# Optimization experiments

Measured on AMD Instinct MI355X. Metric: run time of the kernel, lower is better.

Reference implementation:

```python
import jax, jax.numpy as jnp
from jax import lax
import numpy as np

HID = 512
BATCH = 4096
T = 20
OUT = 1


def setup_inputs() -> dict:
    key = jax.random.key(0)
    ks = jax.random.split(key, 10)
    s = 1.0 / np.sqrt(HID)
    y = jax.random.normal(ks[0], (BATCH, HID), dtype=jnp.float32)
    ts = jnp.arange(T, dtype=jnp.float32) * 0.1  # time grid
    Wi = jax.random.uniform(ks[1], (HID, HID), jnp.float32, -s, s)
    Wf = jax.random.uniform(ks[2], (HID, HID), jnp.float32, -s, s)
    Wg = jax.random.uniform(ks[3], (HID, HID), jnp.float32, -s, s)
    Wo = jax.random.uniform(ks[4], (HID, HID), jnp.float32, -s, s)
    Wout = jax.random.uniform(ks[5], (HID, HID), jnp.float32, -s, s)
    bout = jax.random.uniform(ks[6], (HID,), jnp.float32, -s, s)
    Wfc = jax.random.uniform(ks[7], (OUT, HID), jnp.float32, -s, s)
    bfc = jax.random.uniform(ks[8], (OUT,), jnp.float32, -s, s)
    return {"y": y, "ts": ts, "Wi": Wi, "Wf": Wf, "Wg": Wg, "Wo": Wo,
            "Wout": Wout, "bout": bout, "Wfc": Wfc, "bfc": bfc}


def reference(y, ts, Wi, Wf, Wg, Wo, Wout, bout, Wfc, bfc):
    def odefunc(z):  # z: [B, H]
        i = jax.nn.sigmoid(z @ Wi.T)
        f = jax.nn.sigmoid(z @ Wf.T)  # computed (as in source) but unused in dh
        g = jnp.tanh(z @ Wg.T)
        o = jax.nn.sigmoid(z @ Wo.T)
        dh = o * jnp.tanh(i * g)
        return jax.nn.softmax(dh @ Wout.T + bout, axis=1)

    def euler_step(z, dt):
        z_next = z + dt * odefunc(z)
        return z_next, z_next

    dts = ts[1:] - ts[:-1]
    _, zs = lax.scan(euler_step, y, dts)          # [T-1, B, H]
    zt = jnp.concatenate([y[None], zs], axis=0)   # [T, B, H]
    zt = jax.nn.softmax(zt, axis=2).transpose(1, 0, 2)  # [B, T, H]
    out = zt @ Wfc.T + bfc                        # [B, T, 1]
    return out.squeeze(2)                         # [B, T]
```

## Files before the change

kernel.cpp:

```cpp
#include <hip/hip_runtime.h>
#include <cstdint>
#include <cstddef>

#define HID 512
#define BATCH 4096
#define T_STEPS 20

typedef unsigned short ushort_t;
typedef __attribute__((ext_vector_type(8))) __bf16 bf16x8;
typedef __attribute__((ext_vector_type(4))) float f32x4;

typedef __attribute__((address_space(1))) void gvoid;
typedef __attribute__((address_space(3))) void lvoid;

__device__ __forceinline__ unsigned short f2bf(float f) {
  unsigned int u = __float_as_uint(f);
  u += 0x7FFFu + ((u >> 16) & 1u);
  return (unsigned short)(u >> 16);
}

__device__ __forceinline__ void load_lds16(const void* g, void* l) {
  __builtin_amdgcn_global_load_lds((gvoid*)g, (lvoid*)l, 16, 0, 0);
}

#define WAITV6 do { asm volatile("s_waitcnt vmcnt(6)" ::: "memory"); __builtin_amdgcn_sched_barrier(0); } while (0)
#define WAITV4 do { asm volatile("s_waitcnt vmcnt(4)" ::: "memory"); __builtin_amdgcn_sched_barrier(0); } while (0)
#define WAITV0 do { asm volatile("s_waitcnt vmcnt(0)" ::: "memory"); __builtin_amdgcn_sched_barrier(0); } while (0)

__device__ __forceinline__ float frcp(float x) {
  float r; asm("v_rcp_f32 %0, %1" : "=v"(r) : "v"(x)); return r;
}
__device__ __forceinline__ float fsigm(float x) { return frcp(1.f + __expf(-x)); }
__device__ __forceinline__ float ftanh(float x) { return 1.f - 2.f * frcp(__expf(2.f * x) + 1.f); }

__global__ __launch_bounds__(512) void ode_persistent(
    const float* __restrict__ y,
    const ushort_t* __restrict__ Wcat,
    const ushort_t* __restrict__ WoutB,
    const float* __restrict__ bout,
    const float* __restrict__ Wfc, const float* __restrict__ bfc,
    const float* __restrict__ ts, float* __restrict__ out) {
  __shared__ ushort_t wst[2][8][3072];
  __shared__ ushort_t zbs[64 * 16 * 8];
  __shared__ ushort_t dhs[64 * 16 * 8];
  __shared__ float rmax1[8][16];
  __shared__ float rsum1[8][16];
  __shared__ float rmax2[8][16];
  __shared__ float rsd[8][16][2];
  __shared__ float dts[T_STEPS];

  const int tid = threadIdx.x;
  const int wave = tid >> 6;
  const int lane = tid & 63;
  const int quad = lane >> 4;
  const int l16 = lane & 15;
  const int m0 = blockIdx.x * 16;
  const int wn2 = wave * 64;

  if (tid < T_STEPS - 1) dts[tid] = ts[tid + 1] - ts[tid];

  float boutr[4], wfcr[4];
#pragma unroll
  for (int j = 0; j < 4; ++j) {
    boutr[j] = bout[wn2 + j * 16 + l16];
    wfcr[j] = Wfc[wn2 + j * 16 + l16];
  }
  const float bfc0 = bfc[0];

  ushort_t* const w0 = &wst[0][wave][0];
  ushort_t* const w1 = &wst[1][wave][0];

  int loff1[6];
#pragma unroll
  for (int i = 0; i < 6; ++i) {
    int c = (i & 1) * 8 + (lane >> 3);
    int kc = (lane & 7) ^ (c & 7);
    loff1[i] = (i >> 1) * 262144 + (wave * 16 + c) * 512 + kc * 8;
  }
  int loff2[4];
#pragma unroll
  for (int i = 0; i < 4; ++i) {
    int c = i * 16 + (lane >> 2);
    int kc = (lane & 3) ^ ((lane >> 3) & 3);
    loff2[i] = (wave * 64 + c) * 512 + kc * 8;
  }
  const int x7 = l16 & 7;
  const int x3b = (l16 >> 1) & 3;

  f32x4 zreg[4];
#pragma unroll
  for (int j = 0; j < 4; ++j) {
    int col = wn2 + j * 16 + l16;
    int kp = col >> 3, ce = col & 7;
#pragma unroll
    for (int r = 0; r < 4; ++r) {
      float v = y[(size_t)(m0 + quad * 4 + r) * HID + col];
      zreg[j][r] = v;
      zbs[(kp * 16 + quad * 4 + r) * 8 + ce] = f2bf(v);
    }
  }

  auto proj_out = [&](int tcol) {
    float m2[4];
#pragma unroll
    for (int r = 0; r < 4; ++r) {
      float m = zreg[0][r];
#pragma unroll
      for (int j = 1; j < 4; ++j) m = fmaxf(m, zreg[j][r]);
#pragma unroll
      for (int off = 1; off < 16; off <<= 1) m = fmaxf(m, __shfl_xor(m, off));
      m2[r] = m;
    }
    if (l16 == 0) {
#pragma unroll
      for (int r = 0; r < 4; ++r) rmax2[wave][quad * 4 + r] = m2[r];
    }
    __syncthreads();
#pragma unroll
    for (int r = 0; r < 4; ++r) {
      int row = quad * 4 + r;
      float m = rmax2[0][row];
#pragma unroll
      for (int w = 1; w < 8; ++w) m = fmaxf(m, rmax2[w][row]);
      m2[r] = m;
    }
    float s2[4] = {0.f, 0.f, 0.f, 0.f};
    float dd[4] = {0.f, 0.f, 0.f, 0.f};
#pragma unroll
    for (int j = 0; j < 4; ++j)
#pragma unroll
      for (int r = 0; r < 4; ++r) {
        float e = __expf(zreg[j][r] - m2[r]);
        s2[r] += e;
        dd[r] += e * wfcr[j];
      }
#pragma unroll
    for (int r = 0; r < 4; ++r) {
#pragma unroll
      for (int off = 1; off < 16; off <<= 1) {
        s2[r] += __shfl_xor(s2[r], off);
        dd[r] += __shfl_xor(dd[r], off);
      }
    }
    if (l16 == 0) {
#pragma unroll
      for (int r = 0; r < 4; ++r) {
        rsd[wave][quad * 4 + r][0] = s2[r];
        rsd[wave][quad * 4 + r][1] = dd[r];
      }
    }
    __syncthreads();
    if (wave == 0 && l16 == 0) {
#pragma unroll
      for (int r = 0; r < 4; ++r) {
        int row = quad * 4 + r;
        float ss = 0.f, dv = 0.f;
#pragma unroll
        for (int w = 0; w < 8; ++w) { ss += rsd[w][row][0]; dv += rsd[w][row][1]; }
        out[(size_t)(m0 + row) * T_STEPS + tcol] = dv / ss + bfc0;
      }
    }
    __syncthreads();
  };

  auto stage1n = [&](ushort_t* dst, int nt) {
    const ushort_t* pt = Wcat + ((nt >> 3) << 16) + ((nt & 7) << 6);
#pragma unroll
    for (int i = 0; i < 6; ++i)
      load_lds16(pt + loff1[i], dst + i * 512);
  };
  auto stage2n = [&](ushort_t* dst, int nt) {
    const ushort_t* pt = WoutB + nt * 32;
#pragma unroll
    for (int i = 0; i < 4; ++i)
      load_lds16(pt + loff2[i], dst + i * 512);
  };

  proj_out(0);

  for (int t = 0; t < T_STEPS - 1; ++t) {
    bf16x8 afr[16];
#pragma unroll
    for (int kk = 0; kk < 8; ++kk) {
      afr[2 * kk]     = *(const bf16x8*)&zbs[((kk * 8 + quad) * 16 + l16) * 8];
      afr[2 * kk + 1] = *(const bf16x8*)&zbs[((kk * 8 + 4 + quad) * 16 + l16) * 8];
    }

    stage1n(w0, 0);
#pragma unroll 1
    for (int ht = 0; ht < 4; ++ht) {
      f32x4 a0 = {}, a1 = {}, a2 = {};
#pragma unroll
      for (int kk = 0; kk < 8; ++kk) {
        ushort_t* wc = (kk & 1) ? w1 : w0;
        ushort_t* wn = (kk & 1) ? w0 : w1;
        if (kk < 7) {
          stage1n(wn, ht * 8 + kk + 1); WAITV6;
        } else if (ht < 3) {
          stage1n(wn, ht * 8 + 8); WAITV6;
        } else {
          WAITV0;
        }
        bf16x8 b00 = *(const bf16x8*)&wc[(0 * 128 + l16 * 8 + (quad ^ x7)) * 8];
        bf16x8 b01 = *(const bf16x8*)&wc[(0 * 128 + l16 * 8 + ((quad + 4) ^ x7)) * 8];
        bf16x8 b10 = *(const bf16x8*)&wc[(1 * 128 + l16 * 8 + (quad ^ x7)) * 8];
        bf16x8 b11 = *(const bf16x8*)&wc[(1 * 128 + l16 * 8 + ((quad + 4) ^ x7)) * 8];
        bf16x8 b20 = *(const bf16x8*)&wc[(2 * 128 + l16 * 8 + (quad ^ x7)) * 8];
        bf16x8 b21 = *(const bf16x8*)&wc[(2 * 128 + l16 * 8 + ((quad + 4) ^ x7)) * 8];
        a0 = __builtin_amdgcn_mfma_f32_16x16x32_bf16(afr[2 * kk], b00, a0, 0, 0, 0);
        a0 = __builtin_amdgcn_mfma_f32_16x16x32_bf16(afr[2 * kk + 1], b01, a0, 0, 0, 0);
        a1 = __builtin_amdgcn_mfma_f32_16x16x32_bf16(afr[2 * kk], b10, a1, 0, 0, 0);
        a1 = __builtin_amdgcn_mfma_f32_16x16x32_bf16(afr[2 * kk + 1], b11, a1, 0, 0, 0);
        a2 = __builtin_amdgcn_mfma_f32_16x16x32_bf16(afr[2 * kk], b20, a2, 0, 0, 0);
        a2 = __builtin_amdgcn_mfma_f32_16x16x32_bf16(afr[2 * kk + 1], b21, a2, 0, 0, 0);
      }
      {
        int col = ht * 128 + wave * 16 + l16;
        int kp = col >> 3, ce = col & 7;
#pragma unroll
        for (int r = 0; r < 4; ++r) {
          float gi = fsigm(a0[r]);
          float gg = ftanh(a1[r]);
          float go = fsigm(a2[r]);
          dhs[(kp * 16 + quad * 4 + r) * 8 + ce] = f2bf(go * ftanh(gi * gg));
        }
      }
    }
    __syncthreads();

    f32x4 acc2[4] = {};
    stage2n(w0, 0);
#pragma unroll
    for (int tt = 0; tt < 16; ++tt) {
      ushort_t* wc = (tt & 1) ? w1 : w0;
      ushort_t* wn = (tt & 1) ? w0 : w1;
      if (tt + 1 < 16) { stage2n(wn, tt + 1); WAITV4; } else { WAITV0; }
      bf16x8 afd = *(const bf16x8*)&dhs[((tt * 4 + quad) * 16 + l16) * 8];
#pragma unroll
      for (int j = 0; j < 4; ++j) {
        bf16x8 bf = *(const bf16x8*)&wc[(((j * 16 + l16) * 4) + (quad ^ x3b)) * 8];
        acc2[j] = __builtin_amdgcn_mfma_f32_16x16x32_bf16(afd, bf, acc2[j], 0, 0, 0);
      }
    }

    const float dtv = dts[t];
#pragma unroll
    for (int j = 0; j < 4; ++j)
#pragma unroll
      for (int r = 0; r < 4; ++r) acc2[j][r] += boutr[j];

    float m1[4];
#pragma unroll
    for (int r = 0; r < 4; ++r) {
      float m = acc2[0][r];
#pragma unroll
      for (int j = 1; j < 4; ++j) m = fmaxf(m, acc2[j][r]);
#pragma unroll
      for (int off = 1; off < 16; off <<= 1) m = fmaxf(m, __shfl_xor(m, off));
      m1[r] = m;
    }
    if (l16 == 0) {
#pragma unroll
      for (int r = 0; r < 4; ++r) rmax1[wave][quad * 4 + r] = m1[r];
    }
    __syncthreads();
#pragma unroll
    for (int r = 0; r < 4; ++r) {
      int row = quad * 4 + r;
      float m = rmax1[0][row];
#pragma unroll
      for (int w = 1; w < 8; ++w) m = fmaxf(m, rmax1[w][row]);
      m1[r] = m;
    }

    float s1[4] = {0.f, 0.f, 0.f, 0.f};
#pragma unroll
    for (int j = 0; j < 4; ++j)
#pragma unroll
      for (int r = 0; r < 4; ++r) {
        float e = __expf(acc2[j][r] - m1[r]);
        acc2[j][r] = e;
        s1[r] += e;
      }
#pragma unroll
    for (int r = 0; r < 4; ++r) {
#pragma unroll
      for (int off = 1; off < 16; off <<= 1) s1[r] += __shfl_xor(s1[r], off);
    }
    if (l16 == 0) {
#pragma unroll
      for (int r = 0; r < 4; ++r) rsum1[wave][quad * 4 + r] = s1[r];
    }
    __syncthreads();
    float inv1[4];
#pragma unroll
    for (int r = 0; r < 4; ++r) {
      int row = quad * 4 + r;
      float s = rsum1[0][row];
#pragma unroll
      for (int w = 1; w < 8; ++w) s += rsum1[w][row];
      inv1[r] = 1.f / s;
    }

#pragma unroll
    for (int j = 0; j < 4; ++j) {
      int col = wn2 + j * 16 + l16;
      int kp = col >> 3, ce = col & 7;
#pragma unroll
      for (int r = 0; r < 4; ++r) {
        float zn = zreg[j][r] + dtv * acc2[j][r] * inv1[r];
        zreg[j][r] = zn;
        zbs[(kp * 16 + quad * 4 + r) * 8 + ce] = f2bf(zn);
      }
    }

    proj_out(t + 1);
  }
}

__global__ __launch_bounds__(256) void convw_kernel(
    const float* __restrict__ Wi, const float* __restrict__ Wg,
    const float* __restrict__ Wo, const float* __restrict__ Wout,
    ushort_t* __restrict__ Wcat, ushort_t* __restrict__ WoutB) {
  const int nW = HID * HID;
  int e = (blockIdx.x * 256 + threadIdx.x) * 4;
  const float* src;
  ushort_t* dst;
  if (e < nW)            { src = Wi + e;          dst = Wcat + e; }
  else if (e < 2 * nW)   { src = Wg + (e - nW);   dst = Wcat + e; }
  else if (e < 3 * nW)   { src = Wo + (e - 2*nW); dst = Wcat + e; }
  else                   { src = Wout + (e - 3*nW); dst = WoutB + (e - 3*nW); }
  float4 v = *(const float4*)src;
  union { unsigned short us[4]; uint2 u; } p;
  p.us[0] = f2bf(v.x); p.us[1] = f2bf(v.y); p.us[2] = f2bf(v.z); p.us[3] = f2bf(v.w);
  *(uint2*)dst = p.u;
}

extern "C" void kernel_launch(void* const* d_in, const int* in_sizes, int n_in,
                              void* d_out, int out_size, void* d_ws, size_t ws_size,
                              hipStream_t stream) {
  const float* y    = (const float*)d_in[0];
  const float* ts   = (const float*)d_in[1];
  const float* Wi   = (const float*)d_in[2];
  const float* Wg   = (const float*)d_in[4];
  const float* Wo   = (const float*)d_in[5];
  const float* Wout = (const float*)d_in[6];
  const float* bout = (const float*)d_in[7];
  const float* Wfc  = (const float*)d_in[8];
  const float* bfc  = (const float*)d_in[9];
  float* out = (float*)d_out;

  char* ws = (char*)d_ws;
  ushort_t* Wcat  = (ushort_t*)(ws);
  ushort_t* WoutB = (ushort_t*)(ws + 1572864);

  convw_kernel<<<1024, 256, 0, stream>>>(Wi, Wg, Wo, Wout, Wcat, WoutB);
  ode_persistent<<<256, 512, 0, stream>>>(y, Wcat, WoutB, bout, Wfc, bfc, ts, out);
}
```

Measured before the change: 678.9 us.

## Load weight fragments directly into registers with triple-buffered global loads instead of LDS staging

```diff
diff --git a/kernel.cpp b/kernel.cpp
--- a/kernel.cpp
+++ b/kernel.cpp
@@ -9,9 +9,6 @@
 typedef unsigned short ushort_t;
 typedef __attribute__((ext_vector_type(8))) __bf16 bf16x8;
 typedef __attribute__((ext_vector_type(4))) float f32x4;
-
-typedef __attribute__((address_space(1))) void gvoid;
-typedef __attribute__((address_space(3))) void lvoid;
 
 __device__ __forceinline__ unsigned short f2bf(float f) {
   unsigned int u = __float_as_uint(f);
@@ -19,19 +16,24 @@
   return (unsigned short)(u >> 16);
 }
 
-__device__ __forceinline__ void load_lds16(const void* g, void* l) {
-  __builtin_amdgcn_global_load_lds((gvoid*)g, (lvoid*)l, 16, 0, 0);
-}
-
-#define WAITV6 do { asm volatile("s_waitcnt vmcnt(6)" ::: "memory"); __builtin_amdgcn_sched_barrier(0); } while (0)
-#define WAITV4 do { asm volatile("s_waitcnt vmcnt(4)" ::: "memory"); __builtin_amdgcn_sched_barrier(0); } while (0)
-#define WAITV0 do { asm volatile("s_waitcnt vmcnt(0)" ::: "memory"); __builtin_amdgcn_sched_barrier(0); } while (0)
-
 __device__ __forceinline__ float frcp(float x) {
   float r; asm("v_rcp_f32 %0, %1" : "=v"(r) : "v"(x)); return r;
 }
 __device__ __forceinline__ float fsigm(float x) { return frcp(1.f + __expf(-x)); }
 __device__ __forceinline__ float ftanh(float x) { return 1.f - 2.f * frcp(__expf(2.f * x) + 1.f); }
+
+__device__ __forceinline__ bf16x8 gload(const ushort_t* base, int voff) {
+  bf16x8 r;
+  asm volatile("global_load_dwordx4 %0, %1, %2"
+               : "=v"(r) : "v"(voff), "s"(base) : "memory");
+  return r;
+}
+
+#define WAIT12 do { asm volatile("s_waitcnt vmcnt(12)" ::: "memory"); __builtin_amdgcn_sched_barrier(0); } while (0)
+#define WAIT8  do { asm volatile("s_waitcnt vmcnt(8)"  ::: "memory"); __builtin_amdgcn_sched_barrier(0); } while (0)
+#define WAIT6  do { asm volatile("s_waitcnt vmcnt(6)"  ::: "memory"); __builtin_amdgcn_sched_barrier(0); } while (0)
+#define WAIT4  do { asm volatile("s_waitcnt vmcnt(4)"  ::: "memory"); __builtin_amdgcn_sched_barrier(0); } while (0)
+#define WAIT0  do { asm volatile("s_waitcnt vmcnt(0)"  ::: "memory"); __builtin_amdgcn_sched_barrier(0); } while (0)
 
 __global__ __launch_bounds__(512) void ode_persistent(
     const float* __restrict__ y,
@@ -40,7 +42,6 @@
     const float* __restrict__ bout,
     const float* __restrict__ Wfc, const float* __restrict__ bfc,
     const float* __restrict__ ts, float* __restrict__ out) {
-  __shared__ ushort_t wst[2][8][3072];
   __shared__ ushort_t zbs[64 * 16 * 8];
   __shared__ ushort_t dhs[64 * 16 * 8];
   __shared__ float rmax1[8][16];
@@ -67,25 +68,16 @@
   }
   const float bfc0 = bfc[0];
 
-  ushort_t* const w0 = &wst[0][wave][0];
-  ushort_t* const w1 = &wst[1][wave][0];
-
-  int loff1[6];
+  int voff1[6];
 #pragma unroll
   for (int i = 0; i < 6; ++i) {
-    int c = (i & 1) * 8 + (lane >> 3);
-    int kc = (lane & 7) ^ (c & 7);
-    loff1[i] = (i >> 1) * 262144 + (wave * 16 + c) * 512 + kc * 8;
+    int gate = i >> 1, half = i & 1;
+    voff1[i] = 2 * (gate * 262144 + (wave * 16 + l16) * 512 + half * 32 + quad * 8);
   }
-  int loff2[4];
-#pragma unroll
-  for (int i = 0; i < 4; ++i) {
-    int c = i * 16 + (lane >> 2);
-    int kc = (lane & 3) ^ ((lane >> 3) & 3);
-    loff2[i] = (wave * 64 + c) * 512 + kc * 8;
-  }
-  const int x7 = l16 & 7;
-  const int x3b = (l16 >> 1) & 3;
+  int voff2[4];
+#pragma unroll
+  for (int j = 0; j < 4; ++j)
+    voff2[j] = 2 * ((wave * 64 + j * 16 + l16) * 512 + quad * 8);
 
   f32x4 zreg[4];
 #pragma unroll
@@ -163,19 +155,6 @@
     __syncthreads();
   };
 
-  auto stage1n = [&](ushort_t* dst, int nt) {
-    const ushort_t* pt = Wcat + ((nt >> 3) << 16) + ((nt & 7) << 6);
-#pragma unroll
-    for (int i = 0; i < 6; ++i)
-      load_lds16(pt + loff1[i], dst + i * 512);
-  };
-  auto stage2n = [&](ushort_t* dst, int nt) {
-    const ushort_t* pt = WoutB + nt * 32;
-#pragma unroll
-    for (int i = 0; i < 4; ++i)
-      load_lds16(pt + loff2[i], dst + i * 512);
-  };
-
   proj_out(0);
 
   for (int t = 0; t < T_STEPS - 1; ++t) {
@@ -186,36 +165,37 @@
       afr[2 * kk + 1] = *(const bf16x8*)&zbs[((kk * 8 + 4 + quad) * 16 + l16) * 8];
     }
 
-    stage1n(w0, 0);
-#pragma unroll 1
-    for (int ht = 0; ht < 4; ++ht) {
-      f32x4 a0 = {}, a1 = {}, a2 = {};
-#pragma unroll
-      for (int kk = 0; kk < 8; ++kk) {
-        ushort_t* wc = (kk & 1) ? w1 : w0;
-        ushort_t* wn = (kk & 1) ? w0 : w1;
-        if (kk < 7) {
-          stage1n(wn, ht * 8 + kk + 1); WAITV6;
-        } else if (ht < 3) {
-          stage1n(wn, ht * 8 + 8); WAITV6;
-        } else {
-          WAITV0;
-        }
-        bf16x8 b00 = *(const bf16x8*)&wc[(0 * 128 + l16 * 8 + (quad ^ x7)) * 8];
-        bf16x8 b01 = *(const bf16x8*)&wc[(0 * 128 + l16 * 8 + ((quad + 4) ^ x7)) * 8];
-        bf16x8 b10 = *(const bf16x8*)&wc[(1 * 128 + l16 * 8 + (quad ^ x7)) * 8];
-        bf16x8 b11 = *(const bf16x8*)&wc[(1 * 128 + l16 * 8 + ((quad + 4) ^ x7)) * 8];
-        bf16x8 b20 = *(const bf16x8*)&wc[(2 * 128 + l16 * 8 + (quad ^ x7)) * 8];
-        bf16x8 b21 = *(const bf16x8*)&wc[(2 * 128 + l16 * 8 + ((quad + 4) ^ x7)) * 8];
-        a0 = __builtin_amdgcn_mfma_f32_16x16x32_bf16(afr[2 * kk], b00, a0, 0, 0, 0);
-        a0 = __builtin_amdgcn_mfma_f32_16x16x32_bf16(afr[2 * kk + 1], b01, a0, 0, 0, 0);
-        a1 = __builtin_amdgcn_mfma_f32_16x16x32_bf16(afr[2 * kk], b10, a1, 0, 0, 0);
-        a1 = __builtin_amdgcn_mfma_f32_16x16x32_bf16(afr[2 * kk + 1], b11, a1, 0, 0, 0);
-        a2 = __builtin_amdgcn_mfma_f32_16x16x32_bf16(afr[2 * kk], b20, a2, 0, 0, 0);
-        a2 = __builtin_amdgcn_mfma_f32_16x16x32_bf16(afr[2 * kk + 1], b21, a2, 0, 0, 0);
-      }
+    bf16x8 bb[3][6];
+#pragma unroll
+    for (int p = 0; p < 3; ++p) {
+      const int d = (p >> 3) * 131072 + (p & 7) * 128;
+#pragma unroll
+      for (int i = 0; i < 6; ++i) bb[p][i] = gload(Wcat, voff1[i] + d);
+    }
+    f32x4 a0 = {}, a1 = {}, a2 = {};
+#pragma unroll
+    for (int g = 0; g < 32; ++g) {
+      const int kk = g & 7;
+      if (kk == 0) { a0 = f32x4{}; a1 = f32x4{}; a2 = f32x4{}; }
+      if (g <= 29) { WAIT12; } else if (g == 30) { WAIT6; } else { WAIT0; }
       {
-        int col = ht * 128 + wave * 16 + l16;
+        bf16x8* s = bb[g % 3];
+        a0 = __builtin_amdgcn_mfma_f32_16x16x32_bf16(afr[2 * kk],     s[0], a0, 0, 0, 0);
+        a0 = __builtin_amdgcn_mfma_f32_16x16x32_bf16(afr[2 * kk + 1], s[1], a0, 0, 0, 0);
+        a1 = __builtin_amdgcn_mfma_f32_16x16x32_bf16(afr[2 * kk],     s[2], a1, 0, 0, 0);
+        a1 = __builtin_amdgcn_mfma_f32_16x16x32_bf16(afr[2 * kk + 1], s[3], a1, 0, 0, 0);
+        a2 = __builtin_amdgcn_mfma_f32_16x16x32_bf16(afr[2 * kk],     s[4], a2, 0, 0, 0);
+        a2 = __builtin_amdgcn_mfma_f32_16x16x32_bf16(afr[2 * kk + 1], s[5], a2, 0, 0, 0);
+      }
+      if (g + 3 < 32) {
+        const int n = g + 3;
+        const int d = (n >> 3) * 131072 + (n & 7) * 128;
+        bf16x8* s = bb[n % 3];
+#pragma unroll
+        for (int i = 0; i < 6; ++i) s[i] = gload(Wcat, voff1[i] + d);
+      }
+      if (kk == 7) {
+        int col = (g >> 3) * 128 + wave * 16 + l16;
         int kp = col >> 3, ce = col & 7;
 #pragma unroll
         for (int r = 0; r < 4; ++r) {
@@ -226,20 +206,33 @@
         }
       }
     }
-    __syncthreads();
+
+    bf16x8 b2[3][4];
+#pragma unroll
+    for (int p = 0; p < 3; ++p) {
+#pragma unroll
+      for (int j = 0; j < 4; ++j) b2[p][j] = gload(WoutB, voff2[j] + p * 64);
+    }
+    asm volatile("s_waitcnt lgkmcnt(0)\n\ts_barrier" ::: "memory");
+    __builtin_amdgcn_sched_barrier(0);
 
     f32x4 acc2[4] = {};
-    stage2n(w0, 0);
-#pragma unroll
-    for (int tt = 0; tt < 16; ++tt) {
-      ushort_t* wc = (tt & 1) ? w1 : w0;
-      ushort_t* wn = (tt & 1) ? w0 : w1;
-      if (tt + 1 < 16) { stage2n(wn, tt + 1); WAITV4; } else { WAITV0; }
-      bf16x8 afd = *(const bf16x8*)&dhs[((tt * 4 + quad) * 16 + l16) * 8];
-#pragma unroll
-      for (int j = 0; j < 4; ++j) {
-        bf16x8 bf = *(const bf16x8*)&wc[(((j * 16 + l16) * 4) + (quad ^ x3b)) * 8];
-        acc2[j] = __builtin_amdgcn_mfma_f32_16x16x32_bf16(afd, bf, acc2[j], 0, 0, 0);
+#pragma unroll
+    for (int g = 0; g < 16; ++g) {
+      if (g <= 13) { WAIT8; } else if (g == 14) { WAIT4; } else { WAIT0; }
+      bf16x8 afd = *(const bf16x8*)&dhs[((g * 4 + quad) * 16 + l16) * 8];
+      {
+        bf16x8* s = b2[g % 3];
+        acc2[0] = __builtin_amdgcn_mfma_f32_16x16x32_bf16(afd, s[0], acc2[0], 0, 0, 0);
+        acc2[1] = __builtin_amdgcn_mfma_f32_16x16x32_bf16(afd, s[1], acc2[1], 0, 0, 0);
+        acc2[2] = __builtin_amdgcn_mfma_f32_16x16x32_bf16(afd, s[2], acc2[2], 0, 0, 0);
+        acc2[3] = __builtin_amdgcn_mfma_f32_16x16x32_bf16(afd, s[3], acc2[3], 0, 0, 0);
+      }
+      if (g + 3 < 16) {
+        const int n = g + 3;
+        bf16x8* s = b2[n % 3];
+#pragma unroll
+        for (int j = 0; j < 4; ++j) s[j] = gload(WoutB, voff2[j] + n * 64);
       }
     }
 
```

Result: slower. 1.219 ms (+79.6%).
